# Performance work log

Hardware: AMD Instinct MI355X
Metric: run time of the kernel (lower is better)

Reference implementation:

```python
import jax, jax.numpy as jnp
import numpy as np

B, T, D, H = 4, 2048, 1024, 16
DH = D // H  # 64


def setup_inputs() -> dict:
    key = jax.random.key(0)
    ks = jax.random.split(key, 6)
    s = 0.02
    x = jax.random.normal(ks[0], (B, T, D), dtype=jnp.float32)
    # causal mask: True (1) marks positions to be masked out
    mask = jnp.triu(jnp.ones((T, T), dtype=bool), k=1)[None, None, :, :]
    WQ = jax.random.normal(ks[1], (D, D), dtype=jnp.float32) * s
    WK = jax.random.normal(ks[2], (D, D), dtype=jnp.float32) * s
    WV = jax.random.normal(ks[3], (D, D), dtype=jnp.float32) * s
    WO = jax.random.normal(ks[4], (D, D), dtype=jnp.float32) * s
    z = jnp.zeros((D,), dtype=jnp.float32)
    return {"x": x, "mask": mask, "WQ": WQ, "bQ": z, "WK": WK, "bK": z,
            "WV": WV, "bV": z, "WO": WO, "bO": z}


def reference(x, mask, WQ, bQ, WK, bK, WV, bV, WO, bO):
    Bc, Tc, Dc = x.shape
    def split_heads(t):  # [B,T,D] -> [B,H,T,DH]
        return t.reshape(Bc, Tc, H, DH).transpose(0, 2, 1, 3)
    q = split_heads(x @ WQ + bQ)
    k = split_heads(x @ WK + bK)
    v = split_heads(x @ WV + bV)
    qk = jnp.einsum("bhqd,bhkd->bhqk", q, k) / jnp.sqrt(jnp.float32(DH))
    qk = qk + mask.astype(qk.dtype) * (-1e9)
    attn = jax.nn.softmax(qk, axis=-1)
    ctx = jnp.einsum("bhqk,bhkd->bhqd", attn, v)  # [B,H,T,DH]
    ctx = ctx.transpose(0, 2, 1, 3).reshape(Bc, Tc, Dc)
    return ctx @ WO + bO
```

## Files before the change

### kernel.cpp

```cpp
#include <hip/hip_runtime.h>
#include <hip/hip_bf16.h>
#include <stdint.h>

#define T_SEQ   2048
#define D_MODEL 1024
#define NHEAD   16
#define DHEAD   64
#define BATCH   4
#define MTOK    (BATCH * T_SEQ)

typedef __attribute__((ext_vector_type(4))) float f32x4;
typedef __attribute__((ext_vector_type(16))) float f32x16;
typedef __attribute__((ext_vector_type(8))) short bf16x8;
typedef __attribute__((ext_vector_type(4))) short s16x4;
typedef __attribute__((ext_vector_type(4))) unsigned u32x4;

__device__ __forceinline__ f32x4 mfma16(bf16x8 a, bf16x8 b, f32x4 c) {
  return __builtin_amdgcn_mfma_f32_16x16x32_bf16(a, b, c, 0, 0, 0);
}
__device__ __forceinline__ f32x16 mfma32(bf16x8 a, bf16x8 b, f32x16 c) {
  return __builtin_amdgcn_mfma_f32_32x32x16_bf16(a, b, c, 0, 0, 0);
}

__device__ __forceinline__ short f2bf(float f) {
  __hip_bfloat16 h = __float2bfloat16(f);
  return *reinterpret_cast<short*>(&h);
}

__device__ __forceinline__ unsigned cvtpk(float a, float b) {
  unsigned r;
  asm("v_cvt_pk_bf16_f32 %0, %1, %2" : "=v"(r) : "v"(a), "v"(b));
  return r;
}

union PB { u32x4 u; bf16x8 b; };

#define GLD_LDS16(gp, lp)                                                      \
  __builtin_amdgcn_global_load_lds(                                            \
      (const __attribute__((address_space(1))) void*)(gp),                     \
      (__attribute__((address_space(3))) void*)(lp), 16, 0, 0)

__global__ __launch_bounds__(256) void transpose_w_kernel(
    const float* __restrict__ W0, const float* __restrict__ W1,
    const float* __restrict__ W2, const float* __restrict__ W3,
    short* __restrict__ out)
{
  const int z = blockIdx.z;
  const float* W = (z == 0) ? W0 : (z == 1) ? W1 : (z == 2) ? W2 : W3;
  short* o = out + (size_t)z * D_MODEL * D_MODEL;
  __shared__ float tile[32][33];
  const int n0 = blockIdx.x * 32, k0 = blockIdx.y * 32;
  const int c = threadIdx.x & 31, r = threadIdx.x >> 5;
#pragma unroll
  for (int i = 0; i < 4; i++)
    tile[r + i * 8][c] = W[(size_t)(k0 + r + i * 8) * D_MODEL + n0 + c];
  __syncthreads();
#pragma unroll
  for (int i = 0; i < 4; i++)
    o[(size_t)(n0 + r + i * 8) * D_MODEL + k0 + c] = f2bf(tile[c][r + i * 8]);
}

__global__ __launch_bounds__(256) void cvt_x_kernel(
    const float* __restrict__ x, short* __restrict__ xb)
{
  const size_t i = (size_t)blockIdx.x * 256 + threadIdx.x;
  const float4 a = ((const float4*)x)[i * 2];
  const float4 b = ((const float4*)x)[i * 2 + 1];
  bf16x8 o;
  o[0] = f2bf(a.x); o[1] = f2bf(a.y); o[2] = f2bf(a.z); o[3] = f2bf(a.w);
  o[4] = f2bf(b.x); o[5] = f2bf(b.y); o[6] = f2bf(b.z); o[7] = f2bf(b.w);
  ((bf16x8*)xb)[i] = o;
}

template <int MODE>
__global__ __launch_bounds__(256) void gemm_bt(
    const short* __restrict__ A, const short* __restrict__ Bt,
    const float* __restrict__ bias, void* __restrict__ Cp, float scale)
{
  __shared__ __align__(16) short As[128 * 32];
  __shared__ __align__(16) short Bs[128 * 32];
  const int tid = threadIdx.x, lane = tid & 63, wid = tid >> 6;
  const int wr = wid >> 1, wc = wid & 1;
  const int lg = lane >> 4, ln = lane & 15;
  const int m0 = blockIdx.x * 128, n0 = blockIdx.y * 128;
  const int lrow = lane >> 2, lchunk = lane & 3;

  f32x4 acc[4][4];
#pragma unroll
  for (int i = 0; i < 4; i++)
#pragma unroll
    for (int j = 0; j < 4; j++) acc[i][j] = {0.f, 0.f, 0.f, 0.f};

  for (int k0 = 0; k0 < 1024; k0 += 32) {
#pragma unroll
    for (int s = 0; s < 2; ++s) {
      const int rbase = (wid * 2 + s) * 16;
      const short* gpa = A + (size_t)(m0 + rbase + lrow) * 1024 + k0 + lchunk * 8;
      GLD_LDS16(gpa, As + rbase * 32);
      const short* gpb = Bt + (size_t)(n0 + rbase + lrow) * 1024 + k0 + lchunk * 8;
      GLD_LDS16(gpb, Bs + rbase * 32);
    }
    __syncthreads();
    bf16x8 a[4], b[4];
#pragma unroll
    for (int mi = 0; mi < 4; mi++)
      a[mi] = *(const bf16x8*)(As + (wr * 64 + mi * 16 + ln) * 32 + lg * 8);
#pragma unroll
    for (int ni = 0; ni < 4; ni++)
      b[ni] = *(const bf16x8*)(Bs + (wc * 64 + ni * 16 + ln) * 32 + lg * 8);
#pragma unroll
    for (int mi = 0; mi < 4; mi++)
#pragma unroll
      for (int ni = 0; ni < 4; ni++)
        acc[mi][ni] = mfma16(a[mi], b[ni], acc[mi][ni]);
    __syncthreads();
  }

#pragma unroll
  for (int mi = 0; mi < 4; mi++)
#pragma unroll
    for (int ni = 0; ni < 4; ni++)
#pragma unroll
      for (int r = 0; r < 4; r++) {
        const int row = m0 + wr * 64 + mi * 16 + lg * 4 + r;
        const int col = n0 + wc * 64 + ni * 16 + ln;
        const float v = (acc[mi][ni][r] + bias[col]) * scale;
        if (MODE == 0)
          ((short*)Cp)[(size_t)row * 1024 + col] = f2bf(v);
        else
          ((float*)Cp)[(size_t)row * 1024 + col] = v;
      }
}

__global__ __launch_bounds__(256) void transpose_v_kernel(
    const short* __restrict__ V, short* __restrict__ Vt)
{
  const int bh = blockIdx.y, t0 = blockIdx.x * 64;
  const int b = bh >> 4, h = bh & 15;
  __shared__ __align__(16) short tile[64][72];
  const int tl = threadIdx.x >> 3, c = threadIdx.x & 7;
#pragma unroll
  for (int half = 0; half < 2; half++) {
    const int t = tl + half * 32;
    bf16x8 v = *(const bf16x8*)(V + (size_t)(b * T_SEQ + t0 + t) * 1024 + h * 64 + c * 8);
    *(bf16x8*)&tile[t][c * 8] = v;
  }
  __syncthreads();
#pragma unroll
  for (int half = 0; half < 2; half++) {
    const int dh = tl + half * 32;
    bf16x8 v;
#pragma unroll
    for (int j = 0; j < 8; j++) v[j] = tile[c * 8 + j][dh];
    *(bf16x8*)(Vt + ((size_t)bh * 64 + dh) * T_SEQ + t0 + c * 8) = v;
  }
}

__device__ __forceinline__ void tile_chain(
    const bf16x8* kf0, const bf16x8* kf1,
    const bf16x8* vf0, const bf16x8* vf1,
    const bf16x8* qf,
    f32x16& o0, f32x16& o1, float& m_run, float& l_run,
    const int kv0, const int qw, const int q, const int hi)
{
  f32x16 s0, s1;
#pragma unroll
  for (int i = 0; i < 16; i++) { s0[i] = 0.f; s1[i] = 0.f; }
  __builtin_amdgcn_s_setprio(1);
#pragma unroll
  for (int c = 0; c < 4; c++) s0 = mfma32(kf0[c], qf[c], s0);
#pragma unroll
  for (int c = 0; c < 4; c++) s1 = mfma32(kf1[c], qf[c], s1);
  __builtin_amdgcn_s_setprio(0);

  if (kv0 + 63 > qw) {
    const int qrel = q - kv0 - 4 * hi;
#pragma unroll
    for (int r = 0; r < 16; r++) {
      const int cst = (r & 3) + 8 * (r >> 2);
      if (cst > qrel) s0[r] = -3.0e38f;
      if (cst + 32 > qrel) s1[r] = -3.0e38f;
    }
  }

  float mx;
  {
    float t[8];
#pragma unroll
    for (int i = 0; i < 8; i++)
      t[i] = fmaxf(fmaxf(s0[i], s0[i + 8]), fmaxf(s1[i], s1[i + 8]));
    const float a0 = fmaxf(fmaxf(t[0], t[1]), fmaxf(t[2], t[3]));
    const float a1 = fmaxf(fmaxf(t[4], t[5]), fmaxf(t[6], t[7]));
    mx = fmaxf(a0, a1);
    mx = fmaxf(mx, __shfl_xor(mx, 32));
  }
  const float mn = fmaxf(m_run, mx);
  const float rr = exp2f(m_run - mn);
  m_run = mn;
#pragma unroll
  for (int i = 0; i < 16; i++) s0[i] = exp2f(s0[i] - mn);
#pragma unroll
  for (int i = 0; i < 16; i++) s1[i] = exp2f(s1[i] - mn);
  float ts;
  {
    float t[8];
#pragma unroll
    for (int i = 0; i < 8; i++) t[i] = (s0[i] + s0[i + 8]) + (s1[i] + s1[i + 8]);
    ts = ((t[0] + t[1]) + (t[2] + t[3])) + ((t[4] + t[5]) + (t[6] + t[7]));
    ts += __shfl_xor(ts, 32);
  }
  l_run = l_run * rr + ts;
#pragma unroll
  for (int i = 0; i < 16; i++) { o0[i] *= rr; o1[i] *= rr; }

  const bool low = (hi == 0);
  PB pb[4];
  {
    unsigned c0 = cvtpk(s0[0], s0[1]),   c1 = cvtpk(s0[2], s0[3]);
    unsigned c2 = cvtpk(s0[4], s0[5]),   c3 = cvtpk(s0[6], s0[7]);
    unsigned c4 = cvtpk(s0[8], s0[9]),   c5 = cvtpk(s0[10], s0[11]);
    unsigned c6 = cvtpk(s0[12], s0[13]), c7 = cvtpk(s0[14], s0[15]);
    unsigned d0 = __shfl_xor((int)c0, 32), d1 = __shfl_xor((int)c1, 32);
    unsigned d2 = __shfl_xor((int)c2, 32), d3 = __shfl_xor((int)c3, 32);
    unsigned d4 = __shfl_xor((int)c4, 32), d5 = __shfl_xor((int)c5, 32);
    unsigned d6 = __shfl_xor((int)c6, 32), d7 = __shfl_xor((int)c7, 32);
    pb[0].u = (u32x4){low ? c0 : d2, low ? c1 : d3, low ? d0 : c2, low ? d1 : c3};
    pb[1].u = (u32x4){low ? c4 : d6, low ? c5 : d7, low ? d4 : c6, low ? d5 : c7};
  }
  {
    unsigned c0 = cvtpk(s1[0], s1[1]),   c1 = cvtpk(s1[2], s1[3]);
    unsigned c2 = cvtpk(s1[4], s1[5]),   c3 = cvtpk(s1[6], s1[7]);
    unsigned c4 = cvtpk(s1[8], s1[9]),   c5 = cvtpk(s1[10], s1[11]);
    unsigned c6 = cvtpk(s1[12], s1[13]), c7 = cvtpk(s1[14], s1[15]);
    unsigned d0 = __shfl_xor((int)c0, 32), d1 = __shfl_xor((int)c1, 32);
    unsigned d2 = __shfl_xor((int)c2, 32), d3 = __shfl_xor((int)c3, 32);
    unsigned d4 = __shfl_xor((int)c4, 32), d5 = __shfl_xor((int)c5, 32);
    unsigned d6 = __shfl_xor((int)c6, 32), d7 = __shfl_xor((int)c7, 32);
    pb[2].u = (u32x4){low ? c0 : d2, low ? c1 : d3, low ? d0 : c2, low ? d1 : c3};
    pb[3].u = (u32x4){low ? c4 : d6, low ? c5 : d7, low ? d4 : c6, low ? d5 : c7};
  }

  __builtin_amdgcn_s_setprio(1);
#pragma unroll
  for (int kc = 0; kc < 4; kc++) {
    o0 = mfma32(vf0[kc], pb[kc].b, o0);
    o1 = mfma32(vf1[kc], pb[kc].b, o1);
  }
  __builtin_amdgcn_s_setprio(0);
}

__device__ __forceinline__ void attn_epilogue(
    short* cp, const f32x16& o0, const f32x16& o1, float l_run, int hi)
{
  const float inv = 1.0f / l_run;
#pragma unroll
  for (int g = 0; g < 4; g++) {
    s16x4 w0, w1;
#pragma unroll
    for (int j = 0; j < 4; j++) {
      w0[j] = f2bf(o0[g * 4 + j] * inv);
      w1[j] = f2bf(o1[g * 4 + j] * inv);
    }
    *(s16x4*)(cp + g * 8 + 4 * hi) = w0;
    *(s16x4*)(cp + 32 + g * 8 + 4 * hi) = w1;
  }
}

__global__ __launch_bounds__(256, 2) void attn_fwd(
    const short* __restrict__ Q, const short* __restrict__ K,
    const short* __restrict__ Vt, short* __restrict__ ctx)
{
  const int tid = threadIdx.x, lane = tid & 63, wid = tid >> 6;
  const int hi = lane >> 5, lq = lane & 31;
  const int id = (int)blockIdx.x;
  const int bh = (id & 7) * 8 + ((id >> 3) & 7);
  const int p = (id >> 6) * 4 + wid;
  const int b = bh >> 4, h = bh & 15;

  const int qtA = p, qtB = 63 - p;
  const int qwA = qtA * 32, qwB = qtB * 32;
  const int qA = qwA + lq, qB = qwB + lq;

  bf16x8 qfA[4], qfB[4];
  {
    const short* qpA = Q + (size_t)(b * T_SEQ + qA) * 1024 + h * 64 + hi * 8;
    const short* qpB = Q + (size_t)(b * T_SEQ + qB) * 1024 + h * 64 + hi * 8;
#pragma unroll
    for (int c = 0; c < 4; c++) {
      qfA[c] = *(const bf16x8*)(qpA + c * 16);
      qfB[c] = *(const bf16x8*)(qpB + c * 16);
    }
  }

  f32x16 oA0, oA1, oB0, oB1;
#pragma unroll
  for (int i = 0; i < 16; i++) { oA0[i] = 0.f; oA1[i] = 0.f; oB0[i] = 0.f; oB1[i] = 0.f; }
  float mA = -3.0e38f, lA = 0.f, mB = -3.0e38f, lB = 0.f;

  const int ntA = (qwA + 95) >> 6, ntB = (qwB + 95) >> 6;

  int it = 0;
#pragma unroll 1
  for (; it < ntA; ++it) {
    const int kv0 = it * 64;
    bf16x8 kf0[4], kf1[4], vf0[4], vf1[4];
    {
      const short* kp = K + (size_t)(b * T_SEQ + kv0 + lq) * 1024 + h * 64 + hi * 8;
      const short* vp = Vt + (size_t)(bh * 64 + lq) * T_SEQ + kv0 + hi * 8;
#pragma unroll
      for (int c = 0; c < 4; c++) {
        kf0[c] = *(const bf16x8*)(kp + c * 16);
        kf1[c] = *(const bf16x8*)(kp + 32 * 1024 + c * 16);
        vf0[c] = *(const bf16x8*)(vp + c * 16);
        vf1[c] = *(const bf16x8*)(vp + 32 * T_SEQ + c * 16);
      }
    }
    tile_chain(kf0, kf1, vf0, vf1, qfB, oB0, oB1, mB, lB, kv0, qwB, qB, hi);
    tile_chain(kf0, kf1, vf0, vf1, qfA, oA0, oA1, mA, lA, kv0, qwA, qA, hi);
  }
#pragma unroll 1
  for (; it < ntB; ++it) {
    const int kv0 = it * 64;
    bf16x8 kf0[4], kf1[4], vf0[4], vf1[4];
    {
      const short* kp = K + (size_t)(b * T_SEQ + kv0 + lq) * 1024 + h * 64 + hi * 8;
      const short* vp = Vt + (size_t)(bh * 64 + lq) * T_SEQ + kv0 + hi * 8;
#pragma unroll
      for (int c = 0; c < 4; c++) {
        kf0[c] = *(const bf16x8*)(kp + c * 16);
        kf1[c] = *(const bf16x8*)(kp + 32 * 1024 + c * 16);
        vf0[c] = *(const bf16x8*)(vp + c * 16);
        vf1[c] = *(const bf16x8*)(vp + 32 * T_SEQ + c * 16);
      }
    }
    tile_chain(kf0, kf1, vf0, vf1, qfB, oB0, oB1, mB, lB, kv0, qwB, qB, hi);
  }

  attn_epilogue(ctx + (size_t)(b * T_SEQ + qA) * 1024 + h * 64, oA0, oA1, lA, hi);
  attn_epilogue(ctx + (size_t)(b * T_SEQ + qB) * 1024 + h * 64, oB0, oB1, lB, hi);
}

extern "C" void kernel_launch(void* const* d_in, const int* in_sizes, int n_in,
                              void* d_out, int out_size, void* d_ws, size_t ws_size,
                              hipStream_t stream)
{
  (void)in_sizes; (void)n_in; (void)out_size; (void)ws_size;
  const float* x  = (const float*)d_in[0];
  const float* WQ = (const float*)d_in[2];
  const float* bQ = (const float*)d_in[3];
  const float* WK = (const float*)d_in[4];
  const float* bK = (const float*)d_in[5];
  const float* WV = (const float*)d_in[6];
  const float* bV = (const float*)d_in[7];
  const float* WO = (const float*)d_in[8];
  const float* bO = (const float*)d_in[9];
  float* out = (float*)d_out;

  const size_t MB = 1024ull * 1024ull;
  char* w = (char*)d_ws;
  short* xb = (short*)(w);
  short* Wt = (short*)(w + 16 * MB);
  short* Qb = (short*)(w + 24 * MB);
  short* Kb = (short*)(w + 40 * MB);
  short* Vb = (short*)(w + 56 * MB);
  short* Vt = (short*)(w + 72 * MB);
  short* ctx = xb;

  transpose_w_kernel<<<dim3(32, 32, 4), 256, 0, stream>>>(WQ, WK, WV, WO, Wt);
  cvt_x_kernel<<<dim3(MTOK * D_MODEL / 8 / 256), 256, 0, stream>>>(x, xb);

  const float qscale = 0.125f * 1.4426950408889634f;
  gemm_bt<0><<<dim3(64, 8), 256, 0, stream>>>(xb, Wt + 0 * D_MODEL * D_MODEL, bQ, Qb, qscale);
  gemm_bt<0><<<dim3(64, 8), 256, 0, stream>>>(xb, Wt + 1 * D_MODEL * D_MODEL, bK, Kb, 1.0f);
  gemm_bt<0><<<dim3(64, 8), 256, 0, stream>>>(xb, Wt + 2 * D_MODEL * D_MODEL, bV, Vb, 1.0f);

  transpose_v_kernel<<<dim3(32, 64), 256, 0, stream>>>(Vb, Vt);
  attn_fwd<<<dim3(512), 256, 0, stream>>>(Qb, Kb, Vt, ctx);

  gemm_bt<1><<<dim3(64, 8), 256, 0, stream>>>(ctx, Wt + 3 * D_MODEL * D_MODEL, bO, out, 1.0f);
}
```

Measured before the change: 236.0 us.

## Split attention KV loop across wave pairs and fuse QKV projections into one GEMM

The attention kernel now runs 512 threads per block. Each pair of waves splits the KV tiles of the same query pair by parity, and the two partial softmax states are merged through shared memory before the epilogue. This halves the serial KV loop length per wave and doubles the number of waves, aiming at better latency hiding. The cost is about 80KB of shared memory per block plus a merge step, which may limit occupancy. The three Q/K/V projection GEMMs are also combined into a single launch with a 3x wider grid, removing launch overhead and tail effects.

```diff
diff --git a/kernel.cpp b/kernel.cpp
--- a/kernel.cpp
+++ b/kernel.cpp
@@ -72,10 +72,9 @@
   ((bf16x8*)xb)[i] = o;
 }
 
-template <int MODE>
 __global__ __launch_bounds__(256) void gemm_bt(
     const short* __restrict__ A, const short* __restrict__ Bt,
-    const float* __restrict__ bias, void* __restrict__ Cp, float scale)
+    const float* __restrict__ bias, float* __restrict__ Cp)
 {
   __shared__ __align__(16) short As[128 * 32];
   __shared__ __align__(16) short Bs[128 * 32];
@@ -124,11 +123,73 @@
       for (int r = 0; r < 4; r++) {
         const int row = m0 + wr * 64 + mi * 16 + lg * 4 + r;
         const int col = n0 + wc * 64 + ni * 16 + ln;
+        Cp[(size_t)row * 1024 + col] = acc[mi][ni][r] + bias[col];
+      }
+}
+
+__global__ __launch_bounds__(256) void gemm_qkv(
+    const short* __restrict__ A, const short* __restrict__ Wt,
+    const float* __restrict__ bQ, const float* __restrict__ bK,
+    const float* __restrict__ bV,
+    short* __restrict__ Qb, short* __restrict__ Kb, short* __restrict__ Vb,
+    float qscale)
+{
+  __shared__ __align__(16) short As[128 * 32];
+  __shared__ __align__(16) short Bs[128 * 32];
+  const int tid = threadIdx.x, lane = tid & 63, wid = tid >> 6;
+  const int wr = wid >> 1, wc = wid & 1;
+  const int lg = lane >> 4, ln = lane & 15;
+  const int m0 = blockIdx.x * 128;
+  const int nglob = blockIdx.y * 128;
+  const int seg = blockIdx.y >> 3;
+  const int n0 = nglob & 1023;
+  const short* Bt = Wt + (size_t)nglob * 1024;
+  const float* bias = (seg == 0) ? bQ : (seg == 1) ? bK : bV;
+  short* Cp = (seg == 0) ? Qb : (seg == 1) ? Kb : Vb;
+  const float scale = (seg == 0) ? qscale : 1.0f;
+  const int lrow = lane >> 2, lchunk = lane & 3;
+
+  f32x4 acc[4][4];
+#pragma unroll
+  for (int i = 0; i < 4; i++)
+#pragma unroll
+    for (int j = 0; j < 4; j++) acc[i][j] = {0.f, 0.f, 0.f, 0.f};
+
+  for (int k0 = 0; k0 < 1024; k0 += 32) {
+#pragma unroll
+    for (int s = 0; s < 2; ++s) {
+      const int rbase = (wid * 2 + s) * 16;
+      const short* gpa = A + (size_t)(m0 + rbase + lrow) * 1024 + k0 + lchunk * 8;
+      GLD_LDS16(gpa, As + rbase * 32);
+      const short* gpb = Bt + (size_t)(rbase + lrow) * 1024 + k0 + lchunk * 8;
+      GLD_LDS16(gpb, Bs + rbase * 32);
+    }
+    __syncthreads();
+    bf16x8 a[4], b[4];
+#pragma unroll
+    for (int mi = 0; mi < 4; mi++)
+      a[mi] = *(const bf16x8*)(As + (wr * 64 + mi * 16 + ln) * 32 + lg * 8);
+#pragma unroll
+    for (int ni = 0; ni < 4; ni++)
+      b[ni] = *(const bf16x8*)(Bs + (wc * 64 + ni * 16 + ln) * 32 + lg * 8);
+#pragma unroll
+    for (int mi = 0; mi < 4; mi++)
+#pragma unroll
+      for (int ni = 0; ni < 4; ni++)
+        acc[mi][ni] = mfma16(a[mi], b[ni], acc[mi][ni]);
+    __syncthreads();
+  }
+
+#pragma unroll
+  for (int mi = 0; mi < 4; mi++)
+#pragma unroll
+    for (int ni = 0; ni < 4; ni++)
+#pragma unroll
+      for (int r = 0; r < 4; r++) {
+        const int row = m0 + wr * 64 + mi * 16 + lg * 4 + r;
+        const int col = n0 + wc * 64 + ni * 16 + ln;
         const float v = (acc[mi][ni][r] + bias[col]) * scale;
-        if (MODE == 0)
-          ((short*)Cp)[(size_t)row * 1024 + col] = f2bf(v);
-        else
-          ((float*)Cp)[(size_t)row * 1024 + col] = v;
+        Cp[(size_t)row * 1024 + col] = f2bf(v);
       }
 }
 
@@ -266,7 +327,7 @@
   }
 }
 
-__global__ __launch_bounds__(256, 2) void attn_fwd(
+__global__ __launch_bounds__(512, 4) void attn_fwd(
     const short* __restrict__ Q, const short* __restrict__ K,
     const short* __restrict__ Vt, short* __restrict__ ctx)
 {
@@ -274,8 +335,14 @@
   const int hi = lane >> 5, lq = lane & 31;
   const int id = (int)blockIdx.x;
   const int bh = (id & 7) * 8 + ((id >> 3) & 7);
-  const int p = (id >> 6) * 4 + wid;
+  const int g = id >> 6;
+  const int u = wid >> 1;
+  const int par = wid & 1;
+  const int p = g * 4 + u;
   const int b = bh >> 4, h = bh & 15;
+
+  __shared__ f32x16 osh[4][4][64];
+  __shared__ float mlsh[4][4][64];
 
   const int qtA = p, qtB = 63 - p;
   const int qwA = qtA * 32, qwB = qtB * 32;
@@ -299,9 +366,8 @@
 
   const int ntA = (qwA + 95) >> 6, ntB = (qwB + 95) >> 6;
 
-  int it = 0;
 #pragma unroll 1
-  for (; it < ntA; ++it) {
+  for (int it = par; it < ntB; it += 2) {
     const int kv0 = it * 64;
     bf16x8 kf0[4], kf1[4], vf0[4], vf1[4];
     {
@@ -316,28 +382,37 @@
       }
     }
     tile_chain(kf0, kf1, vf0, vf1, qfB, oB0, oB1, mB, lB, kv0, qwB, qB, hi);
-    tile_chain(kf0, kf1, vf0, vf1, qfA, oA0, oA1, mA, lA, kv0, qwA, qA, hi);
-  }
-#pragma unroll 1
-  for (; it < ntB; ++it) {
-    const int kv0 = it * 64;
-    bf16x8 kf0[4], kf1[4], vf0[4], vf1[4];
+    if (it < ntA)
+      tile_chain(kf0, kf1, vf0, vf1, qfA, oA0, oA1, mA, lA, kv0, qwA, qA, hi);
+  }
+
+  if (par == 0) {
+    osh[u][0][lane] = oA0; osh[u][1][lane] = oA1;
+    osh[u][2][lane] = oB0; osh[u][3][lane] = oB1;
+    mlsh[u][0][lane] = mA; mlsh[u][1][lane] = lA;
+    mlsh[u][2][lane] = mB; mlsh[u][3][lane] = lB;
+  }
+  __syncthreads();
+  if (par == 1) {
     {
-      const short* kp = K + (size_t)(b * T_SEQ + kv0 + lq) * 1024 + h * 64 + hi * 8;
-      const short* vp = Vt + (size_t)(bh * 64 + lq) * T_SEQ + kv0 + hi * 8;
-#pragma unroll
-      for (int c = 0; c < 4; c++) {
-        kf0[c] = *(const bf16x8*)(kp + c * 16);
-        kf1[c] = *(const bf16x8*)(kp + 32 * 1024 + c * 16);
-        vf0[c] = *(const bf16x8*)(vp + c * 16);
-        vf1[c] = *(const bf16x8*)(vp + 32 * T_SEQ + c * 16);
-      }
-    }
-    tile_chain(kf0, kf1, vf0, vf1, qfB, oB0, oB1, mB, lB, kv0, qwB, qB, hi);
-  }
-
-  attn_epilogue(ctx + (size_t)(b * T_SEQ + qA) * 1024 + h * 64, oA0, oA1, lA, hi);
-  attn_epilogue(ctx + (size_t)(b * T_SEQ + qB) * 1024 + h * 64, oB0, oB1, lB, hi);
+      const float m2 = mlsh[u][0][lane], l2 = mlsh[u][1][lane];
+      const float M = fmaxf(mA, m2);
+      const float eS = exp2f(mA - M), eO = exp2f(m2 - M);
+      lA = lA * eS + l2 * eO;
+      oA0 = oA0 * eS + osh[u][0][lane] * eO;
+      oA1 = oA1 * eS + osh[u][1][lane] * eO;
+    }
+    {
+      const float m2 = mlsh[u][2][lane], l2 = mlsh[u][3][lane];
+      const float M = fmaxf(mB, m2);
+      const float eS = exp2f(mB - M), eO = exp2f(m2 - M);
+      lB = lB * eS + l2 * eO;
+      oB0 = oB0 * eS + osh[u][2][lane] * eO;
+      oB1 = oB1 * eS + osh[u][3][lane] * eO;
+    }
+    attn_epilogue(ctx + (size_t)(b * T_SEQ + qA) * 1024 + h * 64, oA0, oA1, lA, hi);
+    attn_epilogue(ctx + (size_t)(b * T_SEQ + qB) * 1024 + h * 64, oB0, oB1, lB, hi);
+  }
 }
 
 extern "C" void kernel_launch(void* const* d_in, const int* in_sizes, int n_in,
@@ -370,12 +445,10 @@
   cvt_x_kernel<<<dim3(MTOK * D_MODEL / 8 / 256), 256, 0, stream>>>(x, xb);
 
   const float qscale = 0.125f * 1.4426950408889634f;
-  gemm_bt<0><<<dim3(64, 8), 256, 0, stream>>>(xb, Wt + 0 * D_MODEL * D_MODEL, bQ, Qb, qscale);
-  gemm_bt<0><<<dim3(64, 8), 256, 0, stream>>>(xb, Wt + 1 * D_MODEL * D_MODEL, bK, Kb, 1.0f);
-  gemm_bt<0><<<dim3(64, 8), 256, 0, stream>>>(xb, Wt + 2 * D_MODEL * D_MODEL, bV, Vb, 1.0f);
+  gemm_qkv<<<dim3(64, 24), 256, 0, stream>>>(xb, Wt, bQ, bK, bV, Qb, Kb, Vb, qscale);
 
   transpose_v_kernel<<<dim3(32, 64), 256, 0, stream>>>(Vb, Vt);
-  attn_fwd<<<dim3(512), 256, 0, stream>>>(Qb, Kb, Vt, ctx);
-
-  gemm_bt<1><<<dim3(64, 8), 256, 0, stream>>>(ctx, Wt + 3 * D_MODEL * D_MODEL, bO, out, 1.0f);
-}
+  attn_fwd<<<dim3(512), 512, 0, stream>>>(Qb, Kb, Vt, ctx);
+
+  gemm_bt<<<dim3(64, 8), 256, 0, stream>>>(ctx, Wt + 3ull * D_MODEL * D_MODEL, bO, out);
+}
```

New measurement: 483.7 us. +105.0%, slower.
